# Kernel optimization log

Measured on AMD Instinct MI355X. Metric: run time of the kernel, lower is better.

## Reference

```python
import jax, jax.numpy as jnp
import numpy as np

DIM = 1024
HEADS = 16
DIM_HEAD = 64
INNER = HEADS * DIM_HEAD  # 1024
MAX_LEN = 4096
BASE = 10000.0
EPS = 1.1920928955078125e-07  # torch.finfo(float32).eps (RMSNorm eps=None default)


def _rope_tables():
    t = np.arange(MAX_LEN, dtype=np.float32)
    inv_freq = 1.0 / (BASE ** (np.arange(0, DIM_HEAD, 2, dtype=np.float32) / DIM_HEAD))
    freqs = np.einsum('i,j->ij', t, inv_freq)          # [max_len, d/2]
    emb = np.concatenate([freqs, freqs], axis=-1)       # [max_len, d]
    return jnp.asarray(np.sin(emb)), jnp.asarray(np.cos(emb))


def setup_inputs() -> dict:
    key = jax.random.key(0)
    ks = jax.random.split(key, 5)
    x = jax.random.normal(ks[0], (2, 2048, DIM), dtype=jnp.float32)
    norm_w = jnp.ones((DIM,), dtype=jnp.float32)
    # store projection weights as [in, out] (transposed torch Linear weight)
    w_qkv = jax.random.normal(ks[1], (DIM, 3 * INNER), dtype=jnp.float32) * (DIM ** -0.5)
    w_o = jax.random.normal(ks[2], (INNER, DIM), dtype=jnp.float32) * (INNER ** -0.5)
    b_o = jax.random.normal(ks[3], (DIM,), dtype=jnp.float32) * 0.01
    sin, cos = _rope_tables()
    return {"x": x, "norm_w": norm_w, "w_qkv": w_qkv, "w_o": w_o, "b_o": b_o,
            "sin": sin, "cos": cos}


def _rotate_half(t):
    t1, t2 = jnp.split(t, 2, axis=-1)
    return jnp.concatenate([-t2, t1], axis=-1)


def _apply_rope(t, sin, cos):
    # t: [b, h, n, d]; sin/cos: [n, d]
    return t * cos + _rotate_half(t) * sin


def reference(x, norm_w, w_qkv, w_o, b_o, sin, cos):
    b, n, _ = x.shape
    # RMSNorm
    xn = x * jax.lax.rsqrt(jnp.mean(x * x, axis=-1, keepdims=True) + EPS) * norm_w
    # QKV projection
    qkv = xn @ w_qkv                                   # [b, n, 3*inner]
    q, k, v = jnp.split(qkv, 3, axis=-1)
    def to_heads(t):
        return t.reshape(b, n, HEADS, DIM_HEAD).transpose(0, 2, 1, 3)  # [b,h,n,d]
    q, k, v = to_heads(q), to_heads(k), to_heads(v)
    s, c = sin[:n], cos[:n]
    q = _apply_rope(q, s, c)
    k = _apply_rope(k, s, c)
    # causal SDPA
    scale = DIM_HEAD ** -0.5
    scores = jnp.einsum('bhqd,bhkd->bhqk', q, k) * scale
    causal = jnp.tril(jnp.ones((n, n), dtype=bool))
    scores = jnp.where(causal, scores, jnp.finfo(scores.dtype).min)
    attn = jax.nn.softmax(scores, axis=-1)
    out = jnp.einsum('bhqk,bhkd->bhqd', attn, v)
    out = out.transpose(0, 2, 1, 3).reshape(b, n, INNER)
    return out @ w_o + b_o
```

## Files before the change

### kernel.cpp

```cpp
#include <hip/hip_runtime.h>
#include <hip/hip_bf16.h>
#include <stdint.h>
#include <stddef.h>

#define NTOK   2048
#define NHEAD  16
#define DHEAD  64
#define DMODEL 1024
#define NROWS  4096
#define NQKV   3072
#define RMS_EPS 1.1920928955078125e-07f
#define QSCALE 0.1803368801111204f

typedef short bf16x8 __attribute__((ext_vector_type(8)));
typedef float f32x4  __attribute__((ext_vector_type(4)));
typedef unsigned short u16x4 __attribute__((ext_vector_type(4)));
typedef unsigned short u16x8 __attribute__((ext_vector_type(8)));

__device__ __forceinline__ unsigned short f2b(float f) {
  unsigned u = __builtin_bit_cast(unsigned, f);
  return (unsigned short)((u + 0x7fffu + ((u >> 16) & 1u)) >> 16);
}

__device__ __forceinline__ unsigned pk2bf(float a, float b) {
  __hip_bfloat162 h = __float22bfloat162_rn(make_float2(a, b));
  unsigned u;
  __builtin_memcpy(&u, &h, 4);
  return u;
}

__device__ __forceinline__ float fexp2(float x) {
#if __has_builtin(__builtin_amdgcn_exp2f)
  return __builtin_amdgcn_exp2f(x);
#else
  float r;
  asm("v_exp_f32 %0, %1" : "=v"(r) : "v"(x));
  return r;
#endif
}

__device__ __forceinline__ void gl16(const void* g, void* l) {
  __builtin_amdgcn_global_load_lds((__attribute__((address_space(1))) void*)g,
                                   (__attribute__((address_space(3))) void*)l,
                                   16, 0, 0);
}

__global__ __launch_bounds__(256) void k_rmsnorm(const float* __restrict__ x,
                                                 const float* __restrict__ w,
                                                 unsigned short* __restrict__ xn) {
  int row = blockIdx.x;
  int t = threadIdx.x;
  float4 v = ((const float4*)(x + (size_t)row * DMODEL))[t];
  float ss = v.x * v.x + v.y * v.y + v.z * v.z + v.w * v.w;
#pragma unroll
  for (int m = 1; m < 64; m <<= 1) ss += __shfl_xor(ss, m, 64);
  __shared__ float red[4];
  if ((t & 63) == 0) red[t >> 6] = ss;
  __syncthreads();
  float tot = (red[0] + red[1]) + (red[2] + red[3]);
  float rs = rsqrtf(tot * (1.0f / DMODEL) + RMS_EPS);
  float4 wv = ((const float4*)w)[t];
  u16x4 o;
  o.x = f2b(v.x * rs * wv.x);
  o.y = f2b(v.y * rs * wv.y);
  o.z = f2b(v.z * rs * wv.z);
  o.w = f2b(v.w * rs * wv.w);
  *(u16x4*)(xn + (size_t)row * DMODEL + t * 4) = o;
}

__global__ __launch_bounds__(256) void k_transpose_bf16(const float* __restrict__ W,
                                                        unsigned short* __restrict__ Wt,
                                                        int K, int Nw) {
  __shared__ float tile[64][65];
  int bk = blockIdx.x * 64;
  int bn = blockIdx.y * 64;
  int t = threadIdx.x;
  int tr = t >> 4;
  int tc = (t & 15) * 4;
#pragma unroll
  for (int rr = 0; rr < 64; rr += 16) {
    float4 v = *(const float4*)&W[(size_t)(bk + tr + rr) * Nw + bn + tc];
    tile[tr + rr][tc + 0] = v.x;
    tile[tr + rr][tc + 1] = v.y;
    tile[tr + rr][tc + 2] = v.z;
    tile[tr + rr][tc + 3] = v.w;
  }
  __syncthreads();
#pragma unroll
  for (int rr = 0; rr < 64; rr += 16) {
    int n = bn + tr + rr;
    u16x4 o;
    o.x = f2b(tile[tc + 0][tr + rr]);
    o.y = f2b(tile[tc + 1][tr + rr]);
    o.z = f2b(tile[tc + 2][tr + rr]);
    o.w = f2b(tile[tc + 3][tr + rr]);
    *(u16x4*)&Wt[(size_t)n * K + bk + tc] = o;
  }
}

__global__ __launch_bounds__(256) void k_qkv_gemm(
    const unsigned short* __restrict__ A, const unsigned short* __restrict__ Bt,
    const float* __restrict__ sin_t, const float* __restrict__ cos_t,
    unsigned short* __restrict__ Qh, unsigned short* __restrict__ Kh,
    unsigned short* __restrict__ VhT) {
  __shared__ unsigned short As[2][128 * 32];
  __shared__ unsigned short Bs[2][128 * 32];
  int bm = blockIdx.x, bn = blockIdx.y;
  int t = threadIdx.x;
  int l = t & 63, w = t >> 6;
  int wr = w >> 1, wc = w & 1;
  int lr = l & 15, lg = l >> 4;
  f32x4 acc[4][4] = {};

  int srow = t >> 2;
  int scho = (t & 3) * 8;
  const unsigned short* Ag = A + (size_t)(bm * 128 + srow) * DMODEL + scho;
  const unsigned short* Bg = Bt + (size_t)(bn * 128 + srow) * DMODEL + scho;

  gl16(Ag, &As[0][t * 8]);
  gl16(Ag + 64 * DMODEL, &As[0][(t + 256) * 8]);
  gl16(Bg, &Bs[0][t * 8]);
  gl16(Bg + 64 * DMODEL, &Bs[0][(t + 256) * 8]);
  __syncthreads();

  for (int i = 0; i < 32; i++) {
    int cur = i & 1, nxt = cur ^ 1;
    if (i < 31) {
      int k1 = (i + 1) * 32;
      gl16(Ag + k1, &As[nxt][t * 8]);
      gl16(Ag + k1 + 64 * DMODEL, &As[nxt][(t + 256) * 8]);
      gl16(Bg + k1, &Bs[nxt][t * 8]);
      gl16(Bg + k1 + 64 * DMODEL, &Bs[nxt][(t + 256) * 8]);
    }
    bf16x8 af[4], bfr[4];
#pragma unroll
    for (int ii = 0; ii < 4; ii++)
      af[ii] = *(const bf16x8*)&As[cur][(wr * 64 + ii * 16 + lr) * 32 + lg * 8];
#pragma unroll
    for (int jj = 0; jj < 4; jj++)
      bfr[jj] = *(const bf16x8*)&Bs[cur][(wc * 64 + jj * 16 + lr) * 32 + lg * 8];
#pragma unroll
    for (int ii = 0; ii < 4; ii++)
#pragma unroll
      for (int jj = 0; jj < 4; jj++)
        acc[ii][jj] = __builtin_amdgcn_mfma_f32_16x16x32_bf16(af[ii], bfr[jj], acc[ii][jj], 0, 0, 0);
    __syncthreads();
  }

  int nc0 = bn * 128 + wc * 64;
  int which = nc0 >> 10;
  int h = (nc0 & 1023) >> 6;
#pragma unroll
  for (int i = 0; i < 4; i++) {
#pragma unroll
    for (int r = 0; r < 4; r++) {
      int m = bm * 128 + wr * 64 + i * 16 + lg * 4 + r;
      int b = m >> 11;
      int n = m & (NTOK - 1);
      if (which == 2) {
#pragma unroll
        for (int j = 0; j < 4; j++) {
          int d = j * 16 + lr;
          VhT[((size_t)((b * NHEAD + h) * DHEAD) + d) * NTOK + n] = f2b(acc[i][j][r]);
        }
      } else {
        size_t obase = ((size_t)(b * NHEAD + h) * NTOK + n) * DHEAD;
        unsigned short* dst = which ? Kh : Qh;
        float qs = which ? 1.0f : QSCALE;
#pragma unroll
        for (int j = 0; j < 2; j++) {
          int d = j * 16 + lr;
          float t1 = acc[i][j][r];
          float t2 = acc[i][j + 2][r];
          float c1 = cos_t[n * DHEAD + d],      s1 = sin_t[n * DHEAD + d];
          float c2 = cos_t[n * DHEAD + d + 32], s2 = sin_t[n * DHEAD + d + 32];
          dst[obase + d]      = f2b((t1 * c1 - t2 * s1) * qs);
          dst[obase + d + 32] = f2b((t2 * c2 + t1 * s2) * qs);
        }
      }
    }
  }
}

#define SL(q, a, b) ((q) | ((a) << 6) | ((b) << 12))
__constant__ int SLOTS[48] = {
  SL(31,0,16), SL(31,16,32), SL(30,15,31), SL(15,0,16),
  SL(30,0,15), SL(29,0,15),  SL(29,15,30), SL(28,14,29), SL(14,0,15),
  SL(28,0,14), SL(27,0,14),  SL(27,14,28), SL(26,13,27), SL(13,0,14),
  SL(26,0,13), SL(25,0,13),  SL(25,13,26), SL(24,12,25), SL(12,0,13),
  SL(24,0,12), SL(23,0,12),  SL(23,12,24), SL(22,11,23), SL(11,0,12),
  SL(22,0,11), SL(21,0,11),  SL(21,11,22), SL(20,10,21), SL(10,0,11),
  SL(20,0,10), SL(19,0,10),  SL(19,10,20), SL(18,9,19),  SL(9,0,10),
  SL(18,0,9),  SL(17,0,9),   SL(17,9,18),  SL(16,8,17),  SL(8,0,9),
  SL(16,0,8),  SL(7,0,8),    SL(6,0,7),    SL(5,0,6),    SL(4,0,5),
  SL(3,0,4),   SL(2,0,3),    SL(1,0,2),    SL(0,0,1)
};

__global__ __launch_bounds__(256, 4) void k_attn(
    const unsigned short* __restrict__ Qh, const unsigned short* __restrict__ Kh,
    const unsigned short* __restrict__ VhT, unsigned short* __restrict__ AO,
    unsigned short* __restrict__ Opart, float* __restrict__ Mpart,
    float* __restrict__ Lpart) {
  int bh = blockIdx.x;
  int sv = SLOTS[blockIdx.y];
  int qt = sv & 63, kt0 = (sv >> 6) & 63, kt1 = sv >> 12;
  bool partial = (kt0 != 0) || (kt1 != qt + 1);
  int half = (kt0 != 0) ? 1 : 0;
  int t = threadIdx.x;
  int l = t & 63, w = t >> 6;
  int lr = l & 15, lg = l >> 4;

  __shared__ unsigned short Ks[2][64 * 64];
  __shared__ unsigned short Vs[2][64 * 64];
  __shared__ unsigned short Ps[4][16 * 64];

  const unsigned short* Qb = Qh  + (size_t)bh * NTOK * DHEAD;
  const unsigned short* Kb = Kh  + (size_t)bh * NTOK * DHEAD;
  const unsigned short* Vb = VhT + (size_t)bh * DHEAD * NTOK;

  int qrow = qt * 64 + w * 16 + lr;
  bf16x8 aq0 = *(const bf16x8*)&Qb[(size_t)qrow * DHEAD + lg * 8];
  bf16x8 aq1 = *(const bf16x8*)&Qb[(size_t)qrow * DHEAD + 32 + lg * 8];

  f32x4 accO[4] = {};
  float mrow = -1e38f;
  float lsum = 0.f;

  int srow = t >> 3;
  int spc  = t & 7;
  int sc0  = (spc ^ (srow & 7)) * 8;
  int sc1  = (spc ^ ((srow + 32) & 7)) * 8;

  int koff[4][2], voff[2][4], poff[2], pwoff[4];
#pragma unroll
  for (int nf = 0; nf < 4; nf++) {
    int krow = nf * 16 + lr;
    koff[nf][0] = krow * 128 + ((lg * 16) ^ ((krow & 7) << 4));
    koff[nf][1] = krow * 128 + ((lg * 16 + 64) ^ ((krow & 7) << 4));
    pwoff[nf] = lr * 128 + ((nf * 32 + lg * 8) ^ ((lr & 7) << 4));
  }
#pragma unroll
  for (int ks = 0; ks < 2; ks++) {
    poff[ks] = lr * 128 + ((lg * 16 + ks * 64) ^ ((lr & 7) << 4));
#pragma unroll
    for (int df = 0; df < 4; df++) {
      int col = df * 16 + lr;
      voff[ks][df] = col * 128 + ((lg * 16 + ks * 64) ^ ((col & 7) << 4));
    }
  }

  {
    int kv0 = kt0 * 64;
    gl16(Kb + (size_t)(kv0 + srow) * DHEAD + sc0, &Ks[0][t * 8]);
    gl16(Kb + (size_t)(kv0 + srow + 32) * DHEAD + sc1, &Ks[0][(t + 256) * 8]);
    gl16(Vb + (size_t)srow * NTOK + kv0 + sc0, &Vs[0][t * 8]);
    gl16(Vb + (size_t)(srow + 32) * NTOK + kv0 + sc1, &Vs[0][(t + 256) * 8]);
  }
  __syncthreads();

  for (int kt = kt0; kt < kt1; ++kt) {
    int cur = (kt - kt0) & 1, nxt = cur ^ 1;
    int kv0 = kt * 64;

    if (kt + 1 < kt1) {
      int kvn = kv0 + 64;
      gl16(Kb + (size_t)(kvn + srow) * DHEAD + sc0, &Ks[nxt][t * 8]);
      gl16(Kb + (size_t)(kvn + srow + 32) * DHEAD + sc1, &Ks[nxt][(t + 256) * 8]);
      gl16(Vb + (size_t)srow * NTOK + kvn + sc0, &Vs[nxt][t * 8]);
      gl16(Vb + (size_t)(srow + 32) * NTOK + kvn + sc1, &Vs[nxt][(t + 256) * 8]);
    }

    const char* kb = (const char*)Ks[cur];
    f32x4 s[4];
#pragma unroll
    for (int nf = 0; nf < 4; nf++) {
      bf16x8 bk0 = *(const bf16x8*)(kb + koff[nf][0]);
      bf16x8 bk1 = *(const bf16x8*)(kb + koff[nf][1]);
      f32x4 z = {};
      z = __builtin_amdgcn_mfma_f32_16x16x32_bf16(bk0, aq0, z, 0, 0, 0);
      s[nf] = __builtin_amdgcn_mfma_f32_16x16x32_bf16(bk1, aq1, z, 0, 0, 0);
    }

    if (kt == qt) {
      int qr = qt * 64 + w * 16 + lr;
#pragma unroll
      for (int nf = 0; nf < 4; nf++)
#pragma unroll
        for (int r = 0; r < 4; r++)
          if (kv0 + nf * 16 + lg * 4 + r > qr) s[nf][r] = -1e30f;
    }

    float t1m = fmaxf(fmaxf(s[0][0], s[0][1]), s[0][2]);
    float t2m = fmaxf(fmaxf(s[0][3], s[1][0]), s[1][1]);
    float t3m = fmaxf(fmaxf(s[1][2], s[1][3]), s[2][0]);
    float t4m = fmaxf(fmaxf(s[2][1], s[2][2]), s[2][3]);
    float t5m = fmaxf(fmaxf(s[3][0], s[3][1]), s[3][2]);
    float pm = fmaxf(fmaxf(fmaxf(t1m, t2m), t3m), fmaxf(fmaxf(t4m, t5m), s[3][3]));
    pm = fmaxf(pm, __shfl_xor(pm, 16, 64));
    pm = fmaxf(pm, __shfl_xor(pm, 32, 64));
    if (__any(pm > mrow + 8.0f)) {
      float mnew = fmaxf(mrow, pm);
      float corr = fexp2(mrow - mnew);
      mrow = mnew;
      lsum *= corr;
      float c0 = __shfl(corr, lg * 4 + 0, 64);
      float c1 = __shfl(corr, lg * 4 + 1, 64);
      float c2 = __shfl(corr, lg * 4 + 2, 64);
      float c3 = __shfl(corr, lg * 4 + 3, 64);
#pragma unroll
      for (int df = 0; df < 4; df++) {
        accO[df][0] *= c0; accO[df][1] *= c1;
        accO[df][2] *= c2; accO[df][3] *= c3;
      }
    }
    {
      float m = mrow;
      float sum = 0.f;
      char* pw = (char*)Ps[w];
#pragma unroll
      for (int nf = 0; nf < 4; nf++) {
        float p0 = fexp2(s[nf][0] - m);
        float p1 = fexp2(s[nf][1] - m);
        float p2 = fexp2(s[nf][2] - m);
        float p3 = fexp2(s[nf][3] - m);
        sum += (p0 + p1) + (p2 + p3);
        unsigned w0 = pk2bf(p0, p1);
        unsigned w1 = pk2bf(p2, p3);
        *(uint64_t*)(pw + pwoff[nf]) = (uint64_t)w0 | ((uint64_t)w1 << 32);
      }
      sum += __shfl_xor(sum, 16, 64);
      sum += __shfl_xor(sum, 32, 64);
      lsum += sum;
    }

    const char* pb = (const char*)Ps[w];
    const char* vb = (const char*)Vs[cur];
#pragma unroll
    for (int ks = 0; ks < 2; ks++) {
      bf16x8 ap = *(const bf16x8*)(pb + poff[ks]);
#pragma unroll
      for (int df = 0; df < 4; df++) {
        bf16x8 bv = *(const bf16x8*)(vb + voff[ks][df]);
        accO[df] = __builtin_amdgcn_mfma_f32_16x16x32_bf16(ap, bv, accO[df], 0, 0, 0);
      }
    }
    __syncthreads();
  }

  if (partial) {
    int pbase = (((bh << 4) + (qt - 16)) << 1) + half;
    if (lg == 0) {
      Mpart[pbase * 64 + w * 16 + lr] = mrow;
      Lpart[pbase * 64 + w * 16 + lr] = lsum;
    }
    unsigned short* Od = Opart + (size_t)pbase * 4096;
#pragma unroll
    for (int df = 0; df < 4; df++)
#pragma unroll
      for (int r = 0; r < 4; r++)
        Od[(w * 16 + lg * 4 + r) * 64 + df * 16 + lr] = f2b(accO[df][r]);
  } else {
    int b = bh >> 4, h = bh & 15;
    float li = 1.0f / lsum;
    float l0 = __shfl(li, lg * 4 + 0, 64);
    float l1 = __shfl(li, lg * 4 + 1, 64);
    float l2 = __shfl(li, lg * 4 + 2, 64);
    float l3 = __shfl(li, lg * 4 + 3, 64);
    int qbase = qt * 64 + w * 16;
#pragma unroll
    for (int df = 0; df < 4; df++) {
      int d = df * 16 + lr;
      size_t ob = ((size_t)(b * NTOK + qbase + lg * 4)) * DMODEL + h * DHEAD + d;
      AO[ob + 0 * DMODEL] = f2b(accO[df][0] * l0);
      AO[ob + 1 * DMODEL] = f2b(accO[df][1] * l1);
      AO[ob + 2 * DMODEL] = f2b(accO[df][2] * l2);
      AO[ob + 3 * DMODEL] = f2b(accO[df][3] * l3);
    }
  }
}

__global__ __launch_bounds__(256) void k_merge(const unsigned short* __restrict__ Opart,
                                               const float* __restrict__ Mpart,
                                               const float* __restrict__ Lpart,
                                               unsigned short* __restrict__ AO) {
  int bh = blockIdx.x, qq = blockIdx.y;
  int t = threadIdx.x;
  int row = t >> 2, d0 = (t & 3) << 4;
  int p0 = ((bh << 4) + qq) << 1;
  float m1 = Mpart[p0 * 64 + row],       l1 = Lpart[p0 * 64 + row];
  float m2 = Mpart[(p0 + 1) * 64 + row], l2 = Lpart[(p0 + 1) * 64 + row];
  float mm = fmaxf(m1, m2);
  float s1 = fexp2(m1 - mm), s2 = fexp2(m2 - mm);
  float li = 1.0f / (l1 * s1 + l2 * s2);
  float a1 = s1 * li, a2 = s2 * li;
  const unsigned short* O1 = Opart + (size_t)p0 * 4096 + row * 64 + d0;
  const unsigned short* O2 = O1 + 4096;
  int qt = 16 + qq;
  int b = bh >> 4, h = bh & 15;
  unsigned short* dst = AO + ((size_t)(b * NTOK + qt * 64 + row)) * DMODEL + h * DHEAD + d0;
#pragma unroll
  for (int c = 0; c < 2; c++) {
    u16x8 v1 = *(const u16x8*)(O1 + c * 8);
    u16x8 v2 = *(const u16x8*)(O2 + c * 8);
    u16x8 o;
#pragma unroll
    for (int e = 0; e < 8; e++) {
      float f1 = __builtin_bit_cast(float, (unsigned)v1[e] << 16);
      float g1 = __builtin_bit_cast(float, (unsigned)v2[e] << 16);
      o[e] = f2b(f1 * a1 + g1 * a2);
    }
    *(u16x8*)(dst + c * 8) = o;
  }
}

__global__ __launch_bounds__(256) void k_out_gemm(
    const unsigned short* __restrict__ A, const unsigned short* __restrict__ Bt,
    const float* __restrict__ bias, float* __restrict__ out) {
  __shared__ unsigned short As[2][128 * 32];
  __shared__ unsigned short Bs[2][64 * 32];
  int bm = blockIdx.x, bn = blockIdx.y;
  int t = threadIdx.x;
  int l = t & 63, w = t >> 6;
  int wr = w >> 1, wc = w & 1;
  int lr = l & 15, lg = l >> 4;
  f32x4 acc[4][2] = {};

  int srow = t >> 2;
  int scho = (t & 3) * 8;
  const unsigned short* Ag = A + (size_t)(bm * 128 + srow) * DMODEL + scho;
  const unsigned short* Bg = Bt + (size_t)(bn * 64 + srow) * DMODEL + scho;

  gl16(Ag, &As[0][t * 8]);
  gl16(Ag + 64 * DMODEL, &As[0][(t + 256) * 8]);
  if (srow < 64) gl16(Bg, &Bs[0][t * 8]);
  __syncthreads();

  for (int i = 0; i < 32; i++) {
    int cur = i & 1, nxt = cur ^ 1;
    if (i < 31) {
      int k1 = (i + 1) * 32;
      gl16(Ag + k1, &As[nxt][t * 8]);
      gl16(Ag + k1 + 64 * DMODEL, &As[nxt][(t + 256) * 8]);
      if (srow < 64) gl16(Bg + k1, &Bs[nxt][t * 8]);
    }
    bf16x8 af[4], bfr[2];
#pragma unroll
    for (int ii = 0; ii < 4; ii++)
      af[ii] = *(const bf16x8*)&As[cur][(wr * 64 + ii * 16 + lr) * 32 + lg * 8];
#pragma unroll
    for (int jj = 0; jj < 2; jj++)
      bfr[jj] = *(const bf16x8*)&Bs[cur][(wc * 32 + jj * 16 + lr) * 32 + lg * 8];
#pragma unroll
    for (int ii = 0; ii < 4; ii++)
#pragma unroll
      for (int jj = 0; jj < 2; jj++)
        acc[ii][jj] = __builtin_amdgcn_mfma_f32_16x16x32_bf16(af[ii], bfr[jj], acc[ii][jj], 0, 0, 0);
    __syncthreads();
  }
  int nc0 = bn * 64 + wc * 32;
#pragma unroll
  for (int i = 0; i < 4; i++)
#pragma unroll
    for (int r = 0; r < 4; r++) {
      int m = bm * 128 + wr * 64 + i * 16 + lg * 4 + r;
      float* orow = out + (size_t)m * DMODEL;
#pragma unroll
      for (int j = 0; j < 2; j++) {
        int col = nc0 + j * 16 + lr;
        orow[col] = acc[i][j][r] + bias[col];
      }
    }
}

extern "C" void kernel_launch(void* const* d_in, const int* in_sizes, int n_in,
                              void* d_out, int out_size, void* d_ws, size_t ws_size,
                              hipStream_t stream) {
  const float* x      = (const float*)d_in[0];
  const float* norm_w = (const float*)d_in[1];
  const float* w_qkv  = (const float*)d_in[2];
  const float* w_o    = (const float*)d_in[3];
  const float* b_o    = (const float*)d_in[4];
  const float* sin_t  = (const float*)d_in[5];
  const float* cos_t  = (const float*)d_in[6];
  float* out = (float*)d_out;

  char* ws = (char*)d_ws;
  unsigned short* xn    = (unsigned short*)(ws + (0u << 20));
  unsigned short* wqkvT = (unsigned short*)(ws + (8u << 20));
  unsigned short* woT   = (unsigned short*)(ws + (14u << 20));
  unsigned short* Qh    = (unsigned short*)(ws + (16u << 20));
  unsigned short* Kh    = (unsigned short*)(ws + (24u << 20));
  unsigned short* VhT   = (unsigned short*)(ws + (32u << 20));
  unsigned short* AO    = (unsigned short*)(ws + (40u << 20));
  unsigned short* Opart = (unsigned short*)(ws + (0u << 20));
  float*          Mpart = (float*)(ws + (8u << 20));
  float*          Lpart = (float*)(ws + (8u << 20) + (1u << 18));

  hipLaunchKernelGGL(k_rmsnorm, dim3(NROWS), dim3(256), 0, stream, x, norm_w, xn);
  hipLaunchKernelGGL(k_transpose_bf16, dim3(16, 48), dim3(256), 0, stream, w_qkv, wqkvT, DMODEL, NQKV);
  hipLaunchKernelGGL(k_transpose_bf16, dim3(16, 16), dim3(256), 0, stream, w_o, woT, DMODEL, DMODEL);
  hipLaunchKernelGGL(k_qkv_gemm, dim3(32, 24), dim3(256), 0, stream, xn, wqkvT, sin_t, cos_t, Qh, Kh, VhT);
  hipLaunchKernelGGL(k_attn, dim3(32, 48), dim3(256), 0, stream, Qh, Kh, VhT, AO, Opart, Mpart, Lpart);
  hipLaunchKernelGGL(k_merge, dim3(32, 16), dim3(256), 0, stream, Opart, Mpart, Lpart, AO);
  hipLaunchKernelGGL(k_out_gemm, dim3(32, 16), dim3(256), 0, stream, AO, woT, b_o, out);
}
```

Before: 120.0 us.

## Triple-buffer LDS staging in QKV and output GEMMs with explicit vmcnt waits

```diff
diff --git a/kernel.cpp b/kernel.cpp
--- a/kernel.cpp
+++ b/kernel.cpp
@@ -98,13 +98,20 @@
   }
 }
 
+#define QSTAGE(b, k0) do {                                   \
+    gl16(Ag + (k0), &As[b][t * 8]);                          \
+    gl16(Ag + (k0) + 64 * DMODEL, &As[b][(t + 256) * 8]);    \
+    gl16(Bg + (k0), &Bs[b][t * 8]);                          \
+    gl16(Bg + (k0) + 64 * DMODEL, &Bs[b][(t + 256) * 8]);    \
+  } while (0)
+
 __global__ __launch_bounds__(256) void k_qkv_gemm(
     const unsigned short* __restrict__ A, const unsigned short* __restrict__ Bt,
     const float* __restrict__ sin_t, const float* __restrict__ cos_t,
     unsigned short* __restrict__ Qh, unsigned short* __restrict__ Kh,
     unsigned short* __restrict__ VhT) {
-  __shared__ unsigned short As[2][128 * 32];
-  __shared__ unsigned short Bs[2][128 * 32];
+  __shared__ unsigned short As[3][128 * 32];
+  __shared__ unsigned short Bs[3][128 * 32];
   int bm = blockIdx.x, bn = blockIdx.y;
   int t = threadIdx.x;
   int l = t & 63, w = t >> 6;
@@ -117,34 +124,28 @@
   const unsigned short* Ag = A + (size_t)(bm * 128 + srow) * DMODEL + scho;
   const unsigned short* Bg = Bt + (size_t)(bn * 128 + srow) * DMODEL + scho;
 
-  gl16(Ag, &As[0][t * 8]);
-  gl16(Ag + 64 * DMODEL, &As[0][(t + 256) * 8]);
-  gl16(Bg, &Bs[0][t * 8]);
-  gl16(Bg + 64 * DMODEL, &Bs[0][(t + 256) * 8]);
-  __syncthreads();
+  QSTAGE(0, 0);
+  QSTAGE(1, 32);
 
   for (int i = 0; i < 32; i++) {
-    int cur = i & 1, nxt = cur ^ 1;
-    if (i < 31) {
-      int k1 = (i + 1) * 32;
-      gl16(Ag + k1, &As[nxt][t * 8]);
-      gl16(Ag + k1 + 64 * DMODEL, &As[nxt][(t + 256) * 8]);
-      gl16(Bg + k1, &Bs[nxt][t * 8]);
-      gl16(Bg + k1 + 64 * DMODEL, &Bs[nxt][(t + 256) * 8]);
-    }
+    int cb = i % 3;
+    if (i < 31) { asm volatile("s_waitcnt vmcnt(4)" ::: "memory"); }
+    else        { asm volatile("s_waitcnt vmcnt(0)" ::: "memory"); }
+    __builtin_amdgcn_s_barrier();
+    __builtin_amdgcn_sched_barrier(0);
+    if (i < 30) QSTAGE((i + 2) % 3, (i + 2) * 32);
     bf16x8 af[4], bfr[4];
 #pragma unroll
     for (int ii = 0; ii < 4; ii++)
-      af[ii] = *(const bf16x8*)&As[cur][(wr * 64 + ii * 16 + lr) * 32 + lg * 8];
+      af[ii] = *(const bf16x8*)&As[cb][(wr * 64 + ii * 16 + lr) * 32 + lg * 8];
 #pragma unroll
     for (int jj = 0; jj < 4; jj++)
-      bfr[jj] = *(const bf16x8*)&Bs[cur][(wc * 64 + jj * 16 + lr) * 32 + lg * 8];
+      bfr[jj] = *(const bf16x8*)&Bs[cb][(wc * 64 + jj * 16 + lr) * 32 + lg * 8];
 #pragma unroll
     for (int ii = 0; ii < 4; ii++)
 #pragma unroll
       for (int jj = 0; jj < 4; jj++)
         acc[ii][jj] = __builtin_amdgcn_mfma_f32_16x16x32_bf16(af[ii], bfr[jj], acc[ii][jj], 0, 0, 0);
-    __syncthreads();
   }
 
   int nc0 = bn * 128 + wc * 64;
@@ -413,11 +414,17 @@
   }
 }
 
+#define OSTAGE(b, k0) do {                                   \
+    gl16(Ag + (k0), &As[b][t * 8]);                          \
+    gl16(Ag + (k0) + 64 * DMODEL, &As[b][(t + 256) * 8]);    \
+    gl16(Bg + (k0), &Bs[b][t * 8]);                          \
+  } while (0)
+
 __global__ __launch_bounds__(256) void k_out_gemm(
     const unsigned short* __restrict__ A, const unsigned short* __restrict__ Bt,
     const float* __restrict__ bias, float* __restrict__ out) {
-  __shared__ unsigned short As[2][128 * 32];
-  __shared__ unsigned short Bs[2][64 * 32];
+  __shared__ unsigned short As[3][128 * 32];
+  __shared__ unsigned short Bs[3][64 * 32];
   int bm = blockIdx.x, bn = blockIdx.y;
   int t = threadIdx.x;
   int l = t & 63, w = t >> 6;
@@ -428,34 +435,39 @@
   int srow = t >> 2;
   int scho = (t & 3) * 8;
   const unsigned short* Ag = A + (size_t)(bm * 128 + srow) * DMODEL + scho;
-  const unsigned short* Bg = Bt + (size_t)(bn * 64 + srow) * DMODEL + scho;
-
-  gl16(Ag, &As[0][t * 8]);
-  gl16(Ag + 64 * DMODEL, &As[0][(t + 256) * 8]);
-  if (srow < 64) gl16(Bg, &Bs[0][t * 8]);
-  __syncthreads();
+  const unsigned short* Bg = Bt + (size_t)(bn * 64 + (t >> 3)) * DMODEL + (t & 7) * 8;
+
+  (void)Bg;
+  const unsigned short* Bg2 = Bt + (size_t)(bn * 64 + srow) * DMODEL + scho;
+#undef OSTAGE
+#define OSTAGE(b, k0) do {                                   \
+    gl16(Ag + (k0), &As[b][t * 8]);                          \
+    gl16(Ag + (k0) + 64 * DMODEL, &As[b][(t + 256) * 8]);    \
+    gl16(Bg2 + (k0), &Bs[b][t * 8]);                         \
+  } while (0)
+
+  OSTAGE(0, 0);
+  OSTAGE(1, 32);
 
   for (int i = 0; i < 32; i++) {
-    int cur = i & 1, nxt = cur ^ 1;
-    if (i < 31) {
-      int k1 = (i + 1) * 32;
-      gl16(Ag + k1, &As[nxt][t * 8]);
-      gl16(Ag + k1 + 64 * DMODEL, &As[nxt][(t + 256) * 8]);
-      if (srow < 64) gl16(Bg + k1, &Bs[nxt][t * 8]);
-    }
+    int cb = i % 3;
+    if (i < 31) { asm volatile("s_waitcnt vmcnt(3)" ::: "memory"); }
+    else        { asm volatile("s_waitcnt vmcnt(0)" ::: "memory"); }
+    __builtin_amdgcn_s_barrier();
+    __builtin_amdgcn_sched_barrier(0);
+    if (i < 30) OSTAGE((i + 2) % 3, (i + 2) * 32);
     bf16x8 af[4], bfr[2];
 #pragma unroll
     for (int ii = 0; ii < 4; ii++)
-      af[ii] = *(const bf16x8*)&As[cur][(wr * 64 + ii * 16 + lr) * 32 + lg * 8];
+      af[ii] = *(const bf16x8*)&As[cb][(wr * 64 + ii * 16 + lr) * 32 + lg * 8];
 #pragma unroll
     for (int jj = 0; jj < 2; jj++)
-      bfr[jj] = *(const bf16x8*)&Bs[cur][(wc * 32 + jj * 16 + lr) * 32 + lg * 8];
+      bfr[jj] = *(const bf16x8*)&Bs[cb][(wc * 32 + jj * 16 + lr) * 32 + lg * 8];
 #pragma unroll
     for (int ii = 0; ii < 4; ii++)
 #pragma unroll
       for (int jj = 0; jj < 2; jj++)
         acc[ii][jj] = __builtin_amdgcn_mfma_f32_16x16x32_bf16(af[ii], bfr[jj], acc[ii][jj], 0, 0, 0);
-    __syncthreads();
   }
   int nc0 = bn * 64 + wc * 32;
 #pragma unroll
```

New measurement: 118.6 us. About the same (-1.2%).
